# Kernel optimization log

Measured on AMD Instinct MI355X. Metric: run time of the kernel, lower is better.

The kernel has to match this reference:

```python
import jax, jax.numpy as jnp
import numpy as np

GAMMA = 0.3
R_PERCENT = 0.2
LAMBDA_PENALTY = 0.5
EPS = 1e-06

B_SZ, N_HEADS, K_FULL = 16, 32, 32768
K_IMG = 16384


def _zscore(x):
    mu = x.mean(axis=-1, keepdims=True)
    std = jnp.sqrt(((x - mu) ** 2).mean(axis=-1, keepdims=True))  # unbiased=False
    return (x - mu) / (std + EPS)


def _topk_binary(scores, k):
    # scores: [B,H] -> binary mask [B,H]; only strictly-positive topk values count
    vals, idx = jax.lax.top_k(scores, k)
    b = jnp.arange(scores.shape[0])[:, None]
    return jnp.zeros_like(scores).at[b, idx].set((vals > 0).astype(scores.dtype))


def setup_inputs() -> dict:
    key = jax.random.key(0)
    k1, k2, k3, k4, k5 = jax.random.split(key, 5)
    attn_logits_last = jax.random.normal(k1, (B_SZ, N_HEADS, K_FULL), dtype=jnp.float32)
    # exactly K_IMG image tokens per row (alternating pattern -> strided gather)
    image_mask = jnp.tile((jnp.arange(K_FULL) % 2 == 0).astype(jnp.int32)[None, :], (B_SZ, 1))
    feat_C = jax.random.normal(k2, (B_SZ, K_IMG), dtype=jnp.float32)
    feat_A = jax.random.normal(k3, (B_SZ, K_IMG), dtype=jnp.float32)
    feat_D = jax.random.normal(k4, (B_SZ, K_IMG), dtype=jnp.float32)
    feat_B = jax.random.normal(k5, (B_SZ, K_IMG), dtype=jnp.float32)
    return {"attn_logits_last": attn_logits_last, "image_mask": image_mask,
            "feat_C": feat_C, "feat_A": feat_A, "feat_D": feat_D, "feat_B": feat_B}


def reference(attn_logits_last, image_mask, feat_C, feat_A, feat_D, feat_B):
    B, H, K_full = attn_logits_last.shape
    K_img = feat_C.shape[1]

    # --- compute_rf ---
    C_t = jax.nn.relu(_zscore(feat_C))
    A_t = jax.nn.sigmoid(_zscore(feat_A))
    D_t = jax.nn.sigmoid(_zscore(feat_D))
    B_t = jax.nn.sigmoid(_zscore(feat_B))
    denom = jnp.maximum(1.0 + LAMBDA_PENALTY * (D_t + B_t), EPS)
    rf = jnp.maximum(C_t * A_t / denom, 0.0)  # [B,K_img]

    # --- align: positions of image tokens (exactly K_img ones per row) ---
    idx = jax.vmap(lambda m: jnp.nonzero(m, size=K_img)[0])(image_mask)  # [B,K_img]

    # --- image-normalized attention ---
    probs_full = jax.nn.softmax(attn_logits_last, axis=-1)
    mask_f = image_mask[:, None, :].astype(attn_logits_last.dtype)  # [B,1,K_full]
    probs_img = probs_full * mask_f
    probs_img_norm = probs_img / jnp.maximum(probs_img.sum(axis=-1, keepdims=True), EPS)
    attn_img_norm = jnp.take_along_axis(probs_img_norm, idx[:, None, :], axis=-1)  # [B,H,K_img]

    # --- dynamic head roles ---
    low_rf = jnp.maximum(1.0 - rf, 0.0)
    s_pos = (attn_img_norm * rf[:, None, :]).sum(axis=-1)   # [B,H]
    s_neg = (attn_img_norm * low_rf[:, None, :]).sum(axis=-1)
    k_heads = min(max(1, int(np.ceil(R_PERCENT * H))), H)
    m_pos = _topk_binary(s_pos, k_heads)
    neg_scores = jnp.where(m_pos > 0, -jnp.inf, s_neg)
    m_neg = _topk_binary(neg_scores, k_heads) * (m_pos == 0).astype(s_pos.dtype)

    # --- delta and scatter back to full logits ---
    delta_img = GAMMA * (m_pos[:, :, None] * rf[:, None, :]
                         - m_neg[:, :, None] * low_rf[:, None, :])  # [B,H,K_img]
    delta_full = jax.vmap(
        lambda d, i: jnp.zeros((H, K_full), attn_logits_last.dtype).at[:, i].set(d)
    )(delta_img, idx)
    delta_full = delta_full * mask_f
    return attn_logits_last + delta_full
```

## Files before the change

### kernel.cpp

```cpp
#include <hip/hip_runtime.h>
#include <math.h>

#define GAMMA 0.3f
#define EPS 1e-6f
#define B_SZ 16
#define NH 32
#define KF 32768
#define KI 16384
#define KHEADS 7

constexpr int OFF_MU   = 0;
constexpr int OFF_SD   = 64;
constexpr int OFF_SPOS = 128;
constexpr int OFF_SNEG = 640;
constexpr int OFF_CP   = 1152;
constexpr int OFF_CN   = 1664;
constexpr int IOFF_BSUM = 2176;
constexpr int OFF_RF   = 4096;
constexpr int OFF_LRF  = OFF_RF  + B_SZ * KI;
constexpr int OFF_RFF  = OFF_LRF + B_SZ * KI;
constexpr int OFF_LRFF = OFF_RFF + B_SZ * KF;

__global__ __launch_bounds__(256) void k_stats(const float* __restrict__ fC,
        const float* __restrict__ fA, const float* __restrict__ fD,
        const float* __restrict__ fB, float* __restrict__ ws) {
    int bid = blockIdx.x;
    int b = bid >> 2, f = bid & 3;
    const float* src;
    if (f == 0) src = fC; else if (f == 1) src = fA; else if (f == 2) src = fD; else src = fB;
    src += (size_t)b * KI;
    int t = threadIdx.x;
    double s = 0.0, s2 = 0.0;
    for (int i = t; i < KI / 4; i += 256) {
        float4 v = ((const float4*)src)[i];
        s  += (double)v.x + (double)v.y + (double)v.z + (double)v.w;
        s2 += (double)v.x * v.x + (double)v.y * v.y + (double)v.z * v.z + (double)v.w * v.w;
    }
    __shared__ double r1[256], r2[256];
    r1[t] = s; r2[t] = s2; __syncthreads();
    for (int off = 128; off > 0; off >>= 1) {
        if (t < off) { r1[t] += r1[t + off]; r2[t] += r2[t + off]; }
        __syncthreads();
    }
    if (t == 0) {
        double mu  = r1[0] * (1.0 / KI);
        double var = fmax(r2[0] * (1.0 / KI) - mu * mu, 0.0);
        ws[OFF_MU + bid] = (float)mu;
        ws[OFF_SD + bid] = (float)(sqrt(var) + (double)EPS);
    }
}

__global__ __launch_bounds__(256) void k_rf_cnt(const float* __restrict__ fC,
        const float* __restrict__ fA, const float* __restrict__ fD,
        const float* __restrict__ fB, const int* __restrict__ mask,
        float* __restrict__ ws) {
    __shared__ int sred[256];
    int blk = blockIdx.x, t = threadIdx.x;
    if (blk < 256) {
        int base = blk * 1024 + t * 4;
        int b = base >> 14;
        const float* mu = ws + OFF_MU + b * 4;
        const float* sd = ws + OFF_SD + b * 4;
        float4 vC = *(const float4*)(fC + base);
        float4 vA = *(const float4*)(fA + base);
        float4 vD = *(const float4*)(fD + base);
        float4 vB = *(const float4*)(fB + base);
        float rf4[4], lrf4[4];
        float c4[4] = {vC.x, vC.y, vC.z, vC.w};
        float a4[4] = {vA.x, vA.y, vA.z, vA.w};
        float d4[4] = {vD.x, vD.y, vD.z, vD.w};
        float b4[4] = {vB.x, vB.y, vB.z, vB.w};
        #pragma unroll
        for (int j = 0; j < 4; ++j) {
            float Ct = fmaxf((c4[j] - mu[0]) / sd[0], 0.f);
            float At = 1.f / (1.f + __expf(-((a4[j] - mu[1]) / sd[1])));
            float Dt = 1.f / (1.f + __expf(-((d4[j] - mu[2]) / sd[2])));
            float Bt = 1.f / (1.f + __expf(-((b4[j] - mu[3]) / sd[3])));
            float denom = fmaxf(1.f + 0.5f * (Dt + Bt), EPS);
            float rf = fmaxf(Ct * At / denom, 0.f);
            rf4[j] = rf;
            lrf4[j] = fmaxf(1.f - rf, 0.f);
        }
        *(float4*)(ws + OFF_RF  + base) = *(float4*)rf4;
        *(float4*)(ws + OFF_LRF + base) = *(float4*)lrf4;
    } else {
        int cblk = blk - 256;
        const int* mrow = mask + (size_t)cblk * 2048;
        int4 m0 = *(const int4*)(mrow + t * 8);
        int4 m1 = *(const int4*)(mrow + t * 8 + 4);
        int cnt = (m0.x != 0) + (m0.y != 0) + (m0.z != 0) + (m0.w != 0)
                + (m1.x != 0) + (m1.y != 0) + (m1.z != 0) + (m1.w != 0);
        sred[t] = cnt; __syncthreads();
        for (int off = 128; off > 0; off >>= 1) {
            if (t < off) sred[t] += sred[t + off];
            __syncthreads();
        }
        if (t == 0) ((int*)ws)[IOFF_BSUM + cblk] = sred[0];
    }
}

__global__ __launch_bounds__(256) void k_expand(const int* __restrict__ mask,
                                                float* __restrict__ ws) {
    int blk = blockIdx.x, t = threadIdx.x;
    int b = blk >> 4, c = blk & 15;
    const int* bsum = (const int*)ws + IOFF_BSUM;
    int boff = 0;
    for (int i = 0; i < c; ++i) boff += bsum[(b << 4) + i];
    const int* mrow = mask + (size_t)blk * 2048;
    int4 m0 = *(const int4*)(mrow + t * 8);
    int4 m1 = *(const int4*)(mrow + t * 8 + 4);
    int mv[8] = {m0.x, m0.y, m0.z, m0.w, m1.x, m1.y, m1.z, m1.w};
    int cnt = 0;
    #pragma unroll
    for (int j = 0; j < 8; ++j) cnt += (mv[j] != 0);
    __shared__ int sc[256];
    sc[t] = cnt; __syncthreads();
    for (int off = 1; off < 256; off <<= 1) {
        int v = (t >= off) ? sc[t - off] : 0;
        __syncthreads();
        sc[t] += v;
        __syncthreads();
    }
    int r = boff + sc[t] - cnt;
    const float* rf  = ws + OFF_RF  + b * KI;
    const float* lrf = ws + OFF_LRF + b * KI;
    float vr[8], vl[8];
    #pragma unroll
    for (int j = 0; j < 8; ++j) {
        if (mv[j]) { vr[j] = rf[r]; vl[j] = lrf[r]; ++r; }
        else       { vr[j] = 0.f;   vl[j] = 0.f; }
    }
    float* rff  = ws + OFF_RFF  + (size_t)blk * 2048 + t * 8;
    float* lrff = ws + OFF_LRFF + (size_t)blk * 2048 + t * 8;
    *(float4*)(rff)      = *(float4*)(vr);
    *(float4*)(rff + 4)  = *(float4*)(vr + 4);
    *(float4*)(lrff)     = *(float4*)(vl);
    *(float4*)(lrff + 4) = *(float4*)(vl + 4);
}

__global__ __launch_bounds__(256) void k_scores(const float* __restrict__ attn,
                                                float* __restrict__ ws) {
    int bh = blockIdx.x;
    int b = bh >> 5;
    const float* xr   = attn + (size_t)bh * KF;
    const float* rff  = ws + OFF_RFF  + (size_t)b * KF;
    const float* lrff = ws + OFF_LRFF + (size_t)b * KF;
    int t = threadIdx.x;
    float S = 0.f, P = 0.f, N = 0.f;
    #pragma unroll 4
    for (int it = 0; it < KF / (256 * 4); ++it) {
        int k = (it * 256 + t) * 4;
        float4 xs = *(const float4*)(xr + k);
        float4 rv = *(const float4*)(rff + k);
        float4 lv = *(const float4*)(lrff + k);
        float xa[4] = {xs.x, xs.y, xs.z, xs.w};
        float ra[4] = {rv.x, rv.y, rv.z, rv.w};
        float la[4] = {lv.x, lv.y, lv.z, lv.w};
        #pragma unroll
        for (int j = 0; j < 4; ++j) {
            float e = __expf(xa[j]);
            S += (ra[j] + la[j] > 0.f) ? e : 0.f;
            P = fmaf(e, ra[j], P);
            N = fmaf(e, la[j], N);
        }
    }
    __shared__ float rs[256], rp[256], rn[256];
    rs[t] = S; rp[t] = P; rn[t] = N;
    __syncthreads();
    for (int off = 128; off > 0; off >>= 1) {
        if (t < off) { rs[t] += rs[t + off]; rp[t] += rp[t + off]; rn[t] += rn[t + off]; }
        __syncthreads();
    }
    if (t == 0) {
        float S0 = rs[0];
        ws[OFF_SPOS + bh] = rp[0] / S0;
        ws[OFF_SNEG + bh] = rn[0] / S0;
    }
}

__global__ __launch_bounds__(64) void k_topk(float* __restrict__ ws) {
    int b = blockIdx.x, t = threadIdx.x;
    __shared__ float v[NH];
    float sp = 0.f;
    if (t < NH) { sp = ws[OFF_SPOS + b * NH + t]; v[t] = sp; }
    __syncthreads();
    bool mpos = false;
    if (t < NH) {
        int cnt = 0;
        for (int h = 0; h < NH; ++h) { float o = v[h]; cnt += (o > sp) || (o == sp && h < t); }
        mpos = (cnt < KHEADS) && (sp > 0.f);
        ws[OFF_CP + b * NH + t] = mpos ? GAMMA : 0.f;
    }
    __syncthreads();
    float nv = -INFINITY;
    if (t < NH) { nv = mpos ? -INFINITY : ws[OFF_SNEG + b * NH + t]; v[t] = nv; }
    __syncthreads();
    if (t < NH) {
        int cnt = 0;
        for (int h = 0; h < NH; ++h) { float o = v[h]; cnt += (o > nv) || (o == nv && h < t); }
        bool mneg = (cnt < KHEADS) && (nv > 0.f) && !mpos;
        ws[OFF_CN + b * NH + t] = mneg ? GAMMA : 0.f;
    }
}

__global__ __launch_bounds__(256) void k_out(const float* __restrict__ attn,
        const float* __restrict__ ws, float* __restrict__ out) {
    unsigned int u = blockIdx.x * 256 + threadIdx.x;
    unsigned int flat = u * 4;
    unsigned int bh = flat >> 15;
    unsigned int b  = bh >> 5;
    unsigned int k  = flat & (KF - 1);
    float gp = ws[OFF_CP + bh], gn = ws[OFF_CN + bh];
    const float* rff  = ws + OFF_RFF  + ((size_t)b << 15);
    const float* lrff = ws + OFF_LRFF + ((size_t)b << 15);
    float4 xs = *(const float4*)(attn + flat);
    float4 rv = *(const float4*)(rff + k);
    float4 lv = *(const float4*)(lrff + k);
    float4 o;
    o.x = xs.x + gp * rv.x - gn * lv.x;
    o.y = xs.y + gp * rv.y - gn * lv.y;
    o.z = xs.z + gp * rv.z - gn * lv.z;
    o.w = xs.w + gp * rv.w - gn * lv.w;
    *(float4*)(out + flat) = o;
}

extern "C" void kernel_launch(void* const* d_in, const int* in_sizes, int n_in,
                              void* d_out, int out_size, void* d_ws, size_t ws_size,
                              hipStream_t stream) {
    const float* attn = (const float*)d_in[0];
    const int*   mask = (const int*)d_in[1];
    const float* fC   = (const float*)d_in[2];
    const float* fA   = (const float*)d_in[3];
    const float* fD   = (const float*)d_in[4];
    const float* fB   = (const float*)d_in[5];
    float* out = (float*)d_out;
    float* ws = (float*)d_ws;

    k_stats <<<B_SZ * 4, 256, 0, stream>>>(fC, fA, fD, fB, ws);
    k_rf_cnt<<<512, 256, 0, stream>>>(fC, fA, fD, fB, mask, ws);
    k_expand<<<256, 256, 0, stream>>>(mask, ws);
    k_scores<<<B_SZ * NH, 256, 0, stream>>>(attn, ws);
    k_topk  <<<B_SZ, 64, 0, stream>>>(ws);
    k_out   <<<(B_SZ * NH * KF / 4) / 256, 256, 0, stream>>>(attn, ws, out);
}
```

Measured before the change: 161.3 us.

## Merge stats with mask count, drop low_rf buffer, fold top-k into output kernel

Runs the feature statistics and the per-chunk mask counting in a single launch. The expanded low_rf buffer is dropped: one buffer holds rf, with -1 marking non-image positions, and low_rf is recomputed on the fly. The score kernel is split into two halves per (b,h) row that combine through atomicAdd, giving 1024 blocks. Head top-k selection moves into every output block, which removes a launch and a full-size read stream, at the cost of redundant per-block top-k work and float atomics whose accumulation order is not deterministic.

```diff
diff --git a/kernel.cpp b/kernel.cpp
--- a/kernel.cpp
+++ b/kernel.cpp
@@ -9,82 +9,47 @@
 #define KI 16384
 #define KHEADS 7
 
-constexpr int OFF_MU   = 0;
-constexpr int OFF_SD   = 64;
-constexpr int OFF_SPOS = 128;
-constexpr int OFF_SNEG = 640;
-constexpr int OFF_CP   = 1152;
-constexpr int OFF_CN   = 1664;
-constexpr int IOFF_BSUM = 2176;
-constexpr int OFF_RF   = 4096;
-constexpr int OFF_LRF  = OFF_RF  + B_SZ * KI;
-constexpr int OFF_RFF  = OFF_LRF + B_SZ * KI;
-constexpr int OFF_LRFF = OFF_RFF + B_SZ * KF;
-
-__global__ __launch_bounds__(256) void k_stats(const float* __restrict__ fC,
-        const float* __restrict__ fA, const float* __restrict__ fD,
-        const float* __restrict__ fB, float* __restrict__ ws) {
-    int bid = blockIdx.x;
-    int b = bid >> 2, f = bid & 3;
-    const float* src;
-    if (f == 0) src = fC; else if (f == 1) src = fA; else if (f == 2) src = fD; else src = fB;
-    src += (size_t)b * KI;
-    int t = threadIdx.x;
-    double s = 0.0, s2 = 0.0;
-    for (int i = t; i < KI / 4; i += 256) {
-        float4 v = ((const float4*)src)[i];
-        s  += (double)v.x + (double)v.y + (double)v.z + (double)v.w;
-        s2 += (double)v.x * v.x + (double)v.y * v.y + (double)v.z * v.z + (double)v.w * v.w;
-    }
-    __shared__ double r1[256], r2[256];
-    r1[t] = s; r2[t] = s2; __syncthreads();
-    for (int off = 128; off > 0; off >>= 1) {
-        if (t < off) { r1[t] += r1[t + off]; r2[t] += r2[t + off]; }
-        __syncthreads();
-    }
-    if (t == 0) {
-        double mu  = r1[0] * (1.0 / KI);
-        double var = fmax(r2[0] * (1.0 / KI) - mu * mu, 0.0);
-        ws[OFF_MU + bid] = (float)mu;
-        ws[OFF_SD + bid] = (float)(sqrt(var) + (double)EPS);
-    }
-}
-
-__global__ __launch_bounds__(256) void k_rf_cnt(const float* __restrict__ fC,
+constexpr int OFF_MU    = 0;
+constexpr int OFF_SD    = 64;
+constexpr int OFF_RAWS  = 128;
+constexpr int OFF_RAWP  = 640;
+constexpr int OFF_RAWN  = 1152;
+constexpr int IOFF_BSUM = 1664;
+constexpr int OFF_RF    = 4096;
+constexpr int OFF_RFF   = OFF_RF + B_SZ * KI;
+
+__global__ __launch_bounds__(256) void k_stats_cnt(const float* __restrict__ fC,
         const float* __restrict__ fA, const float* __restrict__ fD,
         const float* __restrict__ fB, const int* __restrict__ mask,
         float* __restrict__ ws) {
+    __shared__ double r1[256], r2[256];
     __shared__ int sred[256];
-    int blk = blockIdx.x, t = threadIdx.x;
-    if (blk < 256) {
-        int base = blk * 1024 + t * 4;
-        int b = base >> 14;
-        const float* mu = ws + OFF_MU + b * 4;
-        const float* sd = ws + OFF_SD + b * 4;
-        float4 vC = *(const float4*)(fC + base);
-        float4 vA = *(const float4*)(fA + base);
-        float4 vD = *(const float4*)(fD + base);
-        float4 vB = *(const float4*)(fB + base);
-        float rf4[4], lrf4[4];
-        float c4[4] = {vC.x, vC.y, vC.z, vC.w};
-        float a4[4] = {vA.x, vA.y, vA.z, vA.w};
-        float d4[4] = {vD.x, vD.y, vD.z, vD.w};
-        float b4[4] = {vB.x, vB.y, vB.z, vB.w};
-        #pragma unroll
-        for (int j = 0; j < 4; ++j) {
-            float Ct = fmaxf((c4[j] - mu[0]) / sd[0], 0.f);
-            float At = 1.f / (1.f + __expf(-((a4[j] - mu[1]) / sd[1])));
-            float Dt = 1.f / (1.f + __expf(-((d4[j] - mu[2]) / sd[2])));
-            float Bt = 1.f / (1.f + __expf(-((b4[j] - mu[3]) / sd[3])));
-            float denom = fmaxf(1.f + 0.5f * (Dt + Bt), EPS);
-            float rf = fmaxf(Ct * At / denom, 0.f);
-            rf4[j] = rf;
-            lrf4[j] = fmaxf(1.f - rf, 0.f);
-        }
-        *(float4*)(ws + OFF_RF  + base) = *(float4*)rf4;
-        *(float4*)(ws + OFF_LRF + base) = *(float4*)lrf4;
+    int bid = blockIdx.x, t = threadIdx.x;
+    if (bid < 64) {
+        int b = bid >> 2, f = bid & 3;
+        const float* src;
+        if (f == 0) src = fC; else if (f == 1) src = fA; else if (f == 2) src = fD; else src = fB;
+        src += (size_t)b * KI;
+        double s = 0.0, s2 = 0.0;
+        for (int i = t; i < KI / 4; i += 256) {
+            float4 v = ((const float4*)src)[i];
+            s  += (double)v.x + (double)v.y + (double)v.z + (double)v.w;
+            s2 += (double)v.x * v.x + (double)v.y * v.y + (double)v.z * v.z + (double)v.w * v.w;
+        }
+        r1[t] = s; r2[t] = s2; __syncthreads();
+        for (int off = 128; off > 0; off >>= 1) {
+            if (t < off) { r1[t] += r1[t + off]; r2[t] += r2[t + off]; }
+            __syncthreads();
+        }
+        if (t == 0) {
+            double mu  = r1[0] * (1.0 / KI);
+            double var = fmax(r2[0] * (1.0 / KI) - mu * mu, 0.0);
+            ws[OFF_MU + bid] = (float)mu;
+            ws[OFF_SD + bid] = (float)(sqrt(var) + (double)EPS);
+        }
     } else {
-        int cblk = blk - 256;
+        int cblk = bid - 64;
+        if (cblk < 6) ws[OFF_RAWS + cblk * 256 + t] = 0.f;
         const int* mrow = mask + (size_t)cblk * 2048;
         int4 m0 = *(const int4*)(mrow + t * 8);
         int4 m1 = *(const int4*)(mrow + t * 8 + 4);
@@ -97,6 +62,35 @@
         }
         if (t == 0) ((int*)ws)[IOFF_BSUM + cblk] = sred[0];
     }
+}
+
+__global__ __launch_bounds__(256) void k_rf(const float* __restrict__ fC,
+        const float* __restrict__ fA, const float* __restrict__ fD,
+        const float* __restrict__ fB, float* __restrict__ ws) {
+    int blk = blockIdx.x, t = threadIdx.x;
+    int base = blk * 1024 + t * 4;
+    int b = base >> 14;
+    const float* mu = ws + OFF_MU + b * 4;
+    const float* sd = ws + OFF_SD + b * 4;
+    float4 vC = *(const float4*)(fC + base);
+    float4 vA = *(const float4*)(fA + base);
+    float4 vD = *(const float4*)(fD + base);
+    float4 vB = *(const float4*)(fB + base);
+    float rf4[4];
+    float c4[4] = {vC.x, vC.y, vC.z, vC.w};
+    float a4[4] = {vA.x, vA.y, vA.z, vA.w};
+    float d4[4] = {vD.x, vD.y, vD.z, vD.w};
+    float b4[4] = {vB.x, vB.y, vB.z, vB.w};
+    #pragma unroll
+    for (int j = 0; j < 4; ++j) {
+        float Ct = fmaxf((c4[j] - mu[0]) / sd[0], 0.f);
+        float At = 1.f / (1.f + __expf(-((a4[j] - mu[1]) / sd[1])));
+        float Dt = 1.f / (1.f + __expf(-((d4[j] - mu[2]) / sd[2])));
+        float Bt = 1.f / (1.f + __expf(-((b4[j] - mu[3]) / sd[3])));
+        float denom = fmaxf(1.f + 0.5f * (Dt + Bt), EPS);
+        rf4[j] = fmaxf(Ct * At / denom, 0.f);
+    }
+    *(float4*)(ws + OFF_RF + base) = *(float4*)rf4;
 }
 
 __global__ __launch_bounds__(256) void k_expand(const int* __restrict__ mask,
@@ -122,46 +116,42 @@
         __syncthreads();
     }
     int r = boff + sc[t] - cnt;
-    const float* rf  = ws + OFF_RF  + b * KI;
-    const float* lrf = ws + OFF_LRF + b * KI;
-    float vr[8], vl[8];
+    const float* rf = ws + OFF_RF + b * KI;
+    float vr[8];
     #pragma unroll
     for (int j = 0; j < 8; ++j) {
-        if (mv[j]) { vr[j] = rf[r]; vl[j] = lrf[r]; ++r; }
-        else       { vr[j] = 0.f;   vl[j] = 0.f; }
-    }
-    float* rff  = ws + OFF_RFF  + (size_t)blk * 2048 + t * 8;
-    float* lrff = ws + OFF_LRFF + (size_t)blk * 2048 + t * 8;
-    *(float4*)(rff)      = *(float4*)(vr);
-    *(float4*)(rff + 4)  = *(float4*)(vr + 4);
-    *(float4*)(lrff)     = *(float4*)(vl);
-    *(float4*)(lrff + 4) = *(float4*)(vl + 4);
+        if (mv[j]) { vr[j] = rf[r]; ++r; }
+        else       { vr[j] = -1.f; }
+    }
+    float* rff = ws + OFF_RFF + (size_t)blk * 2048 + t * 8;
+    *(float4*)(rff)     = *(float4*)(vr);
+    *(float4*)(rff + 4) = *(float4*)(vr + 4);
 }
 
 __global__ __launch_bounds__(256) void k_scores(const float* __restrict__ attn,
                                                 float* __restrict__ ws) {
-    int bh = blockIdx.x;
+    int g = blockIdx.x, t = threadIdx.x;
+    int bh = g >> 1, half = g & 1;
     int b = bh >> 5;
-    const float* xr   = attn + (size_t)bh * KF;
-    const float* rff  = ws + OFF_RFF  + (size_t)b * KF;
-    const float* lrff = ws + OFF_LRFF + (size_t)b * KF;
-    int t = threadIdx.x;
+    const float* xr  = attn + ((size_t)bh << 15) + ((size_t)half << 14);
+    const float* rff = ws + OFF_RFF + ((size_t)b << 15) + ((size_t)half << 14);
     float S = 0.f, P = 0.f, N = 0.f;
     #pragma unroll 4
-    for (int it = 0; it < KF / (256 * 4); ++it) {
-        int k = (it * 256 + t) * 4;
+    for (int i = 0; i < 16; ++i) {
+        int k = (i * 256 + t) * 4;
         float4 xs = *(const float4*)(xr + k);
         float4 rv = *(const float4*)(rff + k);
-        float4 lv = *(const float4*)(lrff + k);
         float xa[4] = {xs.x, xs.y, xs.z, xs.w};
-        float ra[4] = {rv.x, rv.y, rv.z, rv.w};
-        float la[4] = {lv.x, lv.y, lv.z, lv.w};
+        float va[4] = {rv.x, rv.y, rv.z, rv.w};
         #pragma unroll
         for (int j = 0; j < 4; ++j) {
             float e = __expf(xa[j]);
-            S += (ra[j] + la[j] > 0.f) ? e : 0.f;
-            P = fmaf(e, ra[j], P);
-            N = fmaf(e, la[j], N);
+            bool on = va[j] >= 0.f;
+            float rfv  = fmaxf(va[j], 0.f);
+            float lrfv = on ? fmaxf(1.f - va[j], 0.f) : 0.f;
+            S += on ? e : 0.f;
+            P = fmaf(e, rfv, P);
+            N = fmaf(e, lrfv, N);
         }
     }
     __shared__ float rs[256], rp[256], rn[256];
@@ -172,55 +162,67 @@
         __syncthreads();
     }
     if (t == 0) {
-        float S0 = rs[0];
-        ws[OFF_SPOS + bh] = rp[0] / S0;
-        ws[OFF_SNEG + bh] = rn[0] / S0;
-    }
-}
-
-__global__ __launch_bounds__(64) void k_topk(float* __restrict__ ws) {
-    int b = blockIdx.x, t = threadIdx.x;
-    __shared__ float v[NH];
-    float sp = 0.f;
-    if (t < NH) { sp = ws[OFF_SPOS + b * NH + t]; v[t] = sp; }
-    __syncthreads();
-    bool mpos = false;
-    if (t < NH) {
-        int cnt = 0;
-        for (int h = 0; h < NH; ++h) { float o = v[h]; cnt += (o > sp) || (o == sp && h < t); }
-        mpos = (cnt < KHEADS) && (sp > 0.f);
-        ws[OFF_CP + b * NH + t] = mpos ? GAMMA : 0.f;
-    }
-    __syncthreads();
-    float nv = -INFINITY;
-    if (t < NH) { nv = mpos ? -INFINITY : ws[OFF_SNEG + b * NH + t]; v[t] = nv; }
-    __syncthreads();
-    if (t < NH) {
-        int cnt = 0;
-        for (int h = 0; h < NH; ++h) { float o = v[h]; cnt += (o > nv) || (o == nv && h < t); }
-        bool mneg = (cnt < KHEADS) && (nv > 0.f) && !mpos;
-        ws[OFF_CN + b * NH + t] = mneg ? GAMMA : 0.f;
+        atomicAdd(&ws[OFF_RAWS + bh], rs[0]);
+        atomicAdd(&ws[OFF_RAWP + bh], rp[0]);
+        atomicAdd(&ws[OFF_RAWN + bh], rn[0]);
     }
 }
 
 __global__ __launch_bounds__(256) void k_out(const float* __restrict__ attn,
         const float* __restrict__ ws, float* __restrict__ out) {
-    unsigned int u = blockIdx.x * 256 + threadIdx.x;
-    unsigned int flat = u * 4;
+    unsigned int t = threadIdx.x;
+    unsigned int flat = (blockIdx.x * 256 + t) * 4;
     unsigned int bh = flat >> 15;
     unsigned int b  = bh >> 5;
-    unsigned int k  = flat & (KF - 1);
-    float gp = ws[OFF_CP + bh], gn = ws[OFF_CN + bh];
-    const float* rff  = ws + OFF_RFF  + ((size_t)b << 15);
-    const float* lrff = ws + OFF_LRFF + ((size_t)b << 15);
+    unsigned int h  = bh & 31;
+
+    __shared__ float ssp[NH], snv[NH];
+    __shared__ int smp[NH];
+    __shared__ float s_gp, s_gn;
+    if (t < NH) {
+        float S0 = ws[OFF_RAWS + b * NH + t];
+        ssp[t] = ws[OFF_RAWP + b * NH + t] / S0;
+        snv[t] = ws[OFF_RAWN + b * NH + t] / S0;
+    }
+    __syncthreads();
+    if (t < NH) {
+        float sp = ssp[t];
+        int cnt = 0;
+        for (int j = 0; j < NH; ++j) { float o = ssp[j]; cnt += (o > sp) || (o == sp && (int)j < (int)t); }
+        smp[t] = (cnt < KHEADS) && (sp > 0.f);
+    }
+    __syncthreads();
+    if (t < NH && smp[t]) snv[t] = -INFINITY;
+    __syncthreads();
+    if (t == 0) {
+        float gp = 0.f, gn = 0.f;
+        if (smp[h]) gp = GAMMA;
+        else {
+            float nv = snv[h];
+            int cnt = 0;
+            for (int j = 0; j < NH; ++j) { float o = snv[j]; cnt += (o > nv) || (o == nv && j < (int)h); }
+            if ((cnt < KHEADS) && (nv > 0.f)) gn = GAMMA;
+        }
+        s_gp = gp; s_gn = gn;
+    }
+    __syncthreads();
+
+    float gp = s_gp, gn = s_gn;
+    const float* rff = ws + OFF_RFF + ((size_t)b << 15);
+    unsigned int k = flat & (KF - 1);
     float4 xs = *(const float4*)(attn + flat);
     float4 rv = *(const float4*)(rff + k);
-    float4 lv = *(const float4*)(lrff + k);
-    float4 o;
-    o.x = xs.x + gp * rv.x - gn * lv.x;
-    o.y = xs.y + gp * rv.y - gn * lv.y;
-    o.z = xs.z + gp * rv.z - gn * lv.z;
-    o.w = xs.w + gp * rv.w - gn * lv.w;
+    float va[4] = {rv.x, rv.y, rv.z, rv.w};
+    float xa[4] = {xs.x, xs.y, xs.z, xs.w};
+    float oa[4];
+    #pragma unroll
+    for (int j = 0; j < 4; ++j) {
+        bool on = va[j] >= 0.f;
+        float rfv  = fmaxf(va[j], 0.f);
+        float lrfv = on ? fmaxf(1.f - va[j], 0.f) : 0.f;
+        oa[j] = xa[j] + gp * rfv - gn * lrfv;
+    }
+    float4 o = {oa[0], oa[1], oa[2], oa[3]};
     *(float4*)(out + flat) = o;
 }
 
@@ -236,10 +238,9 @@
     float* out = (float*)d_out;
     float* ws = (float*)d_ws;
 
-    k_stats <<<B_SZ * 4, 256, 0, stream>>>(fC, fA, fD, fB, ws);
-    k_rf_cnt<<<512, 256, 0, stream>>>(fC, fA, fD, fB, mask, ws);
-    k_expand<<<256, 256, 0, stream>>>(mask, ws);
-    k_scores<<<B_SZ * NH, 256, 0, stream>>>(attn, ws);
-    k_topk  <<<B_SZ, 64, 0, stream>>>(ws);
-    k_out   <<<(B_SZ * NH * KF / 4) / 256, 256, 0, stream>>>(attn, ws, out);
-}
+    k_stats_cnt<<<320, 256, 0, stream>>>(fC, fA, fD, fB, mask, ws);
+    k_rf       <<<256, 256, 0, stream>>>(fC, fA, fD, fB, ws);
+    k_expand   <<<256, 256, 0, stream>>>(mask, ws);
+    k_scores   <<<1024, 256, 0, stream>>>(attn, ws);
+    k_out      <<<(B_SZ * NH * KF / 4) / 256, 256, 0, stream>>>(attn, ws, out);
+}
```

Result: faster. 154.0 us (-4.5%).
